# Optimization experiments

Measured on AMD Instinct MI355X. Metric: run time of the kernel, lower is better.

## Reference

```python
import jax, jax.numpy as jnp
import numpy as np

N_NODES = 100000
N_EDGES = 1600000


def setup_inputs() -> dict:
    key = jax.random.key(0)
    k1, k2, k3, k4 = jax.random.split(key, 4)
    x = jax.random.normal(k1, (N_NODES, 16), dtype=jnp.float32)
    edge_index = jax.random.randint(k2, (2, N_EDGES), 0, N_NODES, dtype=jnp.int32)
    # Glorot-ish init for the two GCN layers
    W1 = jax.random.normal(k3, (16, 32), dtype=jnp.float32) * (1.0 / np.sqrt(16))
    b1 = jnp.zeros((32,), dtype=jnp.float32)
    W2 = jax.random.normal(k4, (32, 2), dtype=jnp.float32) * (1.0 / np.sqrt(32))
    b2 = jnp.zeros((2,), dtype=jnp.float32)
    return {"x": x, "edge_index": edge_index, "W1": W1, "b1": b1, "W2": W2, "b2": b2}


def _gcn_conv(x, W, b, src, dst, norm, n_nodes):
    # PyG GCNConv: h = X @ W; aggregate norm * h[src] at dst; add bias.
    h = x @ W                                   # [N, out]
    msg = h[src] * norm[:, None]                # [E+N, out] gather + scale
    out = jax.ops.segment_sum(msg, dst, num_segments=n_nodes)
    return out + b


def reference(x, edge_index, W1, b1, W2, b2):
    n = x.shape[0]
    self_loops = jnp.arange(n, dtype=edge_index.dtype)
    src = jnp.concatenate([edge_index[0], self_loops])  # [E+N]
    dst = jnp.concatenate([edge_index[1], self_loops])
    # Symmetric GCN normalization: deg computed on graph with self-loops
    deg = jax.ops.segment_sum(jnp.ones_like(dst, dtype=x.dtype), dst, num_segments=n)
    dis = jnp.where(deg > 0, jax.lax.rsqrt(deg), 0.0)   # deg^{-1/2}
    norm = dis[src] * dis[dst]                          # [E+N]

    h = jax.nn.relu(_gcn_conv(x, W1, b1, src, dst, norm, n))
    out = _gcn_conv(h, W2, b2, src, dst, norm, n)
    return out
```

## Files before the change

kernel.cpp:

```cpp
#include <hip/hip_runtime.h>
#include <hip/hip_fp16.h>

static constexpr int N  = 100000;
static constexpr int E  = 1600000;
static constexpr int B  = 256;

static constexpr int NBLK  = 250;
static constexpr int CHUNK = E / NBLK;
static constexpr int PERT  = CHUNK / B;
static constexpr int NBUCK = (N + 63) / 64;
static constexpr int NCNT  = NBUCK * NBLK;
static constexpr int NSB   = (NCNT + B - 1) / B;
static constexpr int CAPD1 = 1536;
static constexpr int CAPD2 = 2560;
static constexpr int ROFS_SZ = NBUCK * 64 + 80;

__device__ __forceinline__ int gbase(const int* scanned, const int* bsum, int idx) {
    return scanned[idx] + bsum[idx >> 8];
}


__global__ void kA_hist(const int* __restrict__ dst, int* __restrict__ counts) {
    __shared__ int hist[NBUCK];
    int t = threadIdx.x, blk = blockIdx.x;
    for (int i = t; i < NBUCK; i += B) hist[i] = 0;
    __syncthreads();
    int eb = blk * CHUNK;
#pragma unroll
    for (int k = 0; k < PERT; ++k) {
        int d = dst[eb + k * B + t];
        atomicAdd(&hist[d >> 6], 1);
    }
    __syncthreads();
    for (int b = t; b < NBUCK; b += B) counts[b * NBLK + blk] = hist[b];
}


__global__ void ks1(const int* __restrict__ counts, int* __restrict__ scanned,
                    int* __restrict__ bsum) {
    __shared__ int s[B];
    int t = threadIdx.x;
    int g = blockIdx.x * B + t;
    s[t] = (g < NCNT) ? counts[g] : 0;
    __syncthreads();
    for (int off = 1; off < B; off <<= 1) {
        int v = (t >= off) ? s[t - off] : 0;
        __syncthreads();
        s[t] += v;
        __syncthreads();
    }
    if (g < NCNT) scanned[g] = (t == 0) ? 0 : s[t - 1];
    if (t == B - 1) bsum[blockIdx.x] = s[t];
}

__global__ void ks2(int* __restrict__ bsum) {
    __shared__ int s[1024];
    __shared__ int carry_s;
    int t = threadIdx.x;
    if (t == 0) carry_s = 0;
    __syncthreads();
    for (int base = 0; base < NSB; base += 1024) {
        int idx = base + t;
        s[t] = (idx < NSB) ? bsum[idx] : 0;
        __syncthreads();
        for (int off = 1; off < 1024; off <<= 1) {
            int u = (t >= off) ? s[t - off] : 0;
            __syncthreads();
            s[t] += u;
            __syncthreads();
        }
        int carry = carry_s;
        __syncthreads();
        if (idx < NSB) bsum[idx] = carry + ((t == 0) ? 0 : s[t - 1]);
        if (t == 1023) carry_s = carry + s[1023];
        __syncthreads();
    }
}


__global__ void kC_scatter(const int* __restrict__ src, const int* __restrict__ dst,
                           const int* __restrict__ scanned, const int* __restrict__ bsum,
                           int* __restrict__ packed) {
    __shared__ int lbase[NBUCK];
    __shared__ int cnt2[NBUCK];
    __shared__ int gb[NBUCK];
    __shared__ int partial[B];
    __shared__ int stage[CHUNK];

    int t = threadIdx.x, blk = blockIdx.x;
    for (int i = t; i < NBUCK; i += B) { lbase[i] = 0; cnt2[i] = 0; }
    __syncthreads();

    int eb = blk * CHUNK;
    int ds[PERT], ss[PERT];
#pragma unroll
    for (int k = 0; k < PERT; ++k) {
        int e = eb + k * B + t;
        ds[k] = dst[e];
        ss[k] = src[e];
        atomicAdd(&lbase[ds[k] >> 6], 1);
    }
    __syncthreads();

    int v[8];
    {
        int i0 = 8 * t, sum = 0;
#pragma unroll
        for (int k = 0; k < 8; ++k) {
            v[k] = (i0 + k < NBUCK) ? lbase[i0 + k] : 0;
            sum += v[k];
        }
        partial[t] = sum;
    }
    __syncthreads();
    for (int off = 1; off < B; off <<= 1) {
        int u = (t >= off) ? partial[t - off] : 0;
        __syncthreads();
        partial[t] += u;
        __syncthreads();
    }
    {
        int run = (t == 0) ? 0 : partial[t - 1];
        int i0 = 8 * t;
#pragma unroll
        for (int k = 0; k < 8; ++k) {
            if (i0 + k < NBUCK) lbase[i0 + k] = run;
            run += v[k];
        }
    }
    for (int b = t; b < NBUCK; b += B)
        gb[b] = gbase(scanned, bsum, b * NBLK + blk);
    __syncthreads();

#pragma unroll
    for (int k = 0; k < PERT; ++k) {
        int d = ds[k], b = d >> 6;
        int r = atomicAdd(&cnt2[b], 1);
        stage[lbase[b] + r] = ss[k] | ((d & 63) << 17);
    }
    __syncthreads();

    for (int slot = t; slot < CHUNK; slot += B) {
        int b = 0;
        for (int step = 1024; step; step >>= 1) {
            int nb = b + step;
            if (nb < NBUCK && lbase[nb] <= slot) b = nb;
        }
        packed[gb[b] + (slot - lbase[b])] = stage[slot];
    }
}


__global__ void kD1_sort(const int* __restrict__ packed, const int* __restrict__ scanned,
                         const int* __restrict__ bsum, const float4* __restrict__ x4,
                         int* __restrict__ sorted, int* __restrict__ rofs,
                         __half* __restrict__ xpre) {
    __shared__ int c[64], basec[64], cur[64];
    __shared__ int stage2[CAPD1];
    int t = threadIdx.x, b = blockIdx.x;
    if (t < 64) { c[t] = 0; cur[t] = 0; }
    __syncthreads();

    int e0 = gbase(scanned, bsum, b * NBLK);
    int e1 = (b == NBUCK - 1) ? E : gbase(scanned, bsum, (b + 1) * NBLK);
    int ne = e1 - e0;

    for (int e = e0 + t; e < e1; e += B)
        atomicAdd(&c[packed[e] >> 17], 1);
    __syncthreads();

    if (t < 64) basec[t] = c[t];
    __syncthreads();
    for (int off = 1; off < 64; off <<= 1) {
        int u = (t < 64 && t >= off) ? basec[t - off] : 0;
        __syncthreads();
        if (t < 64) basec[t] += u;
        __syncthreads();
    }
    if (t < 64) basec[t] -= c[t];
    __syncthreads();

    if (ne <= CAPD1) {
        for (int e = e0 + t; e < e1; e += B) {
            int p = packed[e];
            int lo = p >> 17;
            int r = atomicAdd(&cur[lo], 1);
            stage2[basec[lo] + r] = p;
        }
        __syncthreads();
        for (int k = t; k < ne; k += B) sorted[e0 + k] = stage2[k];
    } else {
        for (int e = e0 + t; e < e1; e += B) {
            int p = packed[e];
            int lo = p >> 17;
            int r = atomicAdd(&cur[lo], 1);
            sorted[e0 + basec[lo] + r] = p;
        }
    }

    if (t < 64) rofs[(size_t)b * 64 + t] = e0 + basec[t];
    if (b == NBUCK - 1 && t < 80) rofs[NBUCK * 64 + t] = E;

    int nbase = b * 64;
    {
        int n = t >> 2, j = t & 3;
        int node = nbase + n;
        if (node < N) {
            float d = rsqrtf((float)(c[n] + 1));
            float4 vv = x4[(size_t)node * 4 + j];
            ushort4 pk;
            pk.x = __half_as_ushort(__float2half(vv.x * d));
            pk.y = __half_as_ushort(__float2half(vv.y * d));
            pk.z = __half_as_ushort(__float2half(vv.z * d));
            pk.w = __half_as_ushort(__float2half(vv.w * d));
            *(ushort4*)(xpre + (size_t)node * 16 + j * 4) = pk;
        }
    }
}


__global__ void kD2_agg(const __half* __restrict__ xpre, const int* __restrict__ sorted,
                        const int* __restrict__ rofs, const float* __restrict__ W1,
                        const float* __restrict__ b1, const float* __restrict__ W2,
                        float2* __restrict__ hpre) {
    __shared__ float acc[128 * 17];
    __shared__ float sW1[512], sb1[32], sW2[64];
    __shared__ int stageE[CAPD2];
    int t = threadIdx.x;
    int nb0 = blockIdx.x * 128;
    for (int i = t; i < 512; i += B) sW1[i] = W1[i];
    if (t < 32) sb1[t] = b1[t];
    if (t < 64) sW2[t] = W2[t];

    int r0 = rofs[nb0];
    int rend = rofs[nb0 + 128];
    int rlen = rend - r0;
    bool useL = (rlen <= CAPD2);
    if (useL) for (int k = t; k < rlen; k += B) stageE[k] = sorted[r0 + k];
    __syncthreads();

    int nl = t >> 1, h = t & 1;
    int n = nb0 + nl;
    if (n < N) {
        int rs = rofs[n], re = rofs[n + 1];
        float a0, a1, a2, a3, a4, a5, a6, a7;
        {
            int4 w = *(const int4*)(xpre + (size_t)n * 16 + h * 8);
            float2 q0 = __half22float2(*(__half2*)&w.x);
            float2 q1 = __half22float2(*(__half2*)&w.y);
            float2 q2 = __half22float2(*(__half2*)&w.z);
            float2 q3 = __half22float2(*(__half2*)&w.w);
            a0 = q0.x; a1 = q0.y; a2 = q1.x; a3 = q1.y;
            a4 = q2.x; a5 = q2.y; a6 = q3.x; a7 = q3.y;
        }
        auto add8 = [&](int4 w) {
            float2 q0 = __half22float2(*(__half2*)&w.x);
            float2 q1 = __half22float2(*(__half2*)&w.y);
            float2 q2 = __half22float2(*(__half2*)&w.z);
            float2 q3 = __half22float2(*(__half2*)&w.w);
            a0 += q0.x; a1 += q0.y; a2 += q1.x; a3 += q1.y;
            a4 += q2.x; a5 += q2.y; a6 += q3.x; a7 += q3.y;
        };
        int k = rs;
        for (; k + 4 <= re; k += 4) {
            int w0, w1, w2, w3;
            if (useL) {
                w0 = stageE[k - r0]; w1 = stageE[k + 1 - r0];
                w2 = stageE[k + 2 - r0]; w3 = stageE[k + 3 - r0];
            } else {
                w0 = sorted[k]; w1 = sorted[k + 1];
                w2 = sorted[k + 2]; w3 = sorted[k + 3];
            }
            int4 v0 = *(const int4*)(xpre + (size_t)(w0 & 0x1FFFF) * 16 + h * 8);
            int4 v1 = *(const int4*)(xpre + (size_t)(w1 & 0x1FFFF) * 16 + h * 8);
            int4 v2 = *(const int4*)(xpre + (size_t)(w2 & 0x1FFFF) * 16 + h * 8);
            int4 v3 = *(const int4*)(xpre + (size_t)(w3 & 0x1FFFF) * 16 + h * 8);
            add8(v0); add8(v1); add8(v2); add8(v3);
        }
        for (; k < re; ++k) {
            int w = useL ? stageE[k - r0] : sorted[k];
            add8(*(const int4*)(xpre + (size_t)(w & 0x1FFFF) * 16 + h * 8));
        }
        float* row = acc + nl * 17 + h * 8;
        row[0] = a0; row[1] = a1; row[2] = a2; row[3] = a3;
        row[4] = a4; row[5] = a5; row[6] = a6; row[7] = a7;
    }
    __syncthreads();

    if (t < 128) {
        int n2 = nb0 + t;
        if (n2 < N) {
            int deg = rofs[n2 + 1] - rofs[n2];
            float d = rsqrtf((float)(deg + 1));
            const float* row = acc + t * 17;
            float xi[16];
#pragma unroll
            for (int k = 0; k < 16; ++k) xi[k] = row[k] * d;
            float o0 = 0.f, o1 = 0.f;
#pragma unroll
            for (int c = 0; c < 32; ++c) {
                float hh = sb1[c];
#pragma unroll
                for (int k = 0; k < 16; ++k) hh = fmaf(xi[k], sW1[k * 32 + c], hh);
                hh = fmaxf(hh, 0.f);
                o0 = fmaf(hh, sW2[c * 2 + 0], o0);
                o1 = fmaf(hh, sW2[c * 2 + 1], o1);
            }
            hpre[n2] = make_float2(d * o0, d * o1);
        }
    }
}


__global__ void kF_l2(const float2* __restrict__ hpre, const int* __restrict__ sorted,
                      const int* __restrict__ rofs, const float* __restrict__ b2,
                      float2* __restrict__ out) {
    int n = blockIdx.x * B + threadIdx.x;
    if (n >= N) return;
    int rs = rofs[n], re = rofs[n + 1];
    float2 self = hpre[n];
    float o0 = self.x, o1 = self.y;
    int k = rs;
    for (; k + 4 <= re; k += 4) {
        int w0 = sorted[k], w1 = sorted[k + 1], w2 = sorted[k + 2], w3 = sorted[k + 3];
        float2 v0 = hpre[w0 & 0x1FFFF];
        float2 v1 = hpre[w1 & 0x1FFFF];
        float2 v2 = hpre[w2 & 0x1FFFF];
        float2 v3 = hpre[w3 & 0x1FFFF];
        o0 += (v0.x + v1.x) + (v2.x + v3.x);
        o1 += (v0.y + v1.y) + (v2.y + v3.y);
    }
    for (; k < re; ++k) {
        float2 v = hpre[sorted[k] & 0x1FFFF];
        o0 += v.x; o1 += v.y;
    }
    float d = rsqrtf((float)(re - rs + 1));
    out[n] = make_float2(fmaf(d, o0, b2[0]), fmaf(d, o1, b2[1]));
}


extern "C" void kernel_launch(void* const* d_in, const int* in_sizes, int n_in,
                              void* d_out, int out_size, void* d_ws, size_t ws_size,
                              hipStream_t stream) {
    const float* x  = (const float*)d_in[0];
    const int*   ei = (const int*)d_in[1];
    const float* W1 = (const float*)d_in[2];
    const float* b1 = (const float*)d_in[3];
    const float* W2 = (const float*)d_in[4];
    const float* b2 = (const float*)d_in[5];

    const int* src = ei;
    const int* dst = ei + E;

    int*    packed  = (int*)d_ws;
    int*    sorted  = packed + E;
    int*    counts  = sorted + E;
    int*    scanned = counts + (size_t)NSB * B;
    int*    bsum    = scanned + (size_t)NSB * B;
    int*    rofs    = bsum + 2048;
    float*  hpre    = (float*)(rofs + 100112);
    __half* xpre    = (__half*)(hpre + 2 * (size_t)N);

    kA_hist<<<NBLK, B, 0, stream>>>(dst, counts);
    ks1<<<NSB, B, 0, stream>>>(counts, scanned, bsum);
    ks2<<<1, 1024, 0, stream>>>(bsum);
    kC_scatter<<<NBLK, B, 0, stream>>>(src, dst, scanned, bsum, packed);
    kD1_sort<<<NBUCK, B, 0, stream>>>(packed, scanned, bsum, (const float4*)x,
                                      sorted, rofs, xpre);
    kD2_agg<<<(NBUCK + 1) / 2, B, 0, stream>>>(xpre, sorted, rofs, W1, b1, W2,
                                               (float2*)hpre);
    kF_l2<<<(N + B - 1) / B, B, 0, stream>>>((const float2*)hpre, sorted, rofs, b2,
                                             (float2*)d_out);
}
```

Before: 153.5 us.

## Replace scan-based bucket sort with fixed-capacity slabs and atomic cursors

Result: faster. 131.4 us (-14.4%).

```diff
diff --git a/kernel.cpp b/kernel.cpp
--- a/kernel.cpp
+++ b/kernel.cpp
@@ -7,113 +7,43 @@
 
 static constexpr int NBLK  = 250;
 static constexpr int CHUNK = E / NBLK;
-static constexpr int PERT  = CHUNK / B;
+static constexpr int BC    = 1024;
 static constexpr int NBUCK = (N + 63) / 64;
-static constexpr int NCNT  = NBUCK * NBLK;
-static constexpr int NSB   = (NCNT + B - 1) / B;
-static constexpr int CAPD1 = 1536;
-static constexpr int CAPD2 = 2560;
-static constexpr int ROFS_SZ = NBUCK * 64 + 80;
-
-__device__ __forceinline__ int gbase(const int* scanned, const int* bsum, int idx) {
-    return scanned[idx] + bsum[idx >> 8];
-}
-
-
-__global__ void kA_hist(const int* __restrict__ dst, int* __restrict__ counts) {
-    __shared__ int hist[NBUCK];
+static constexpr int SLAB  = 1536;
+
+
+__global__ __launch_bounds__(BC, 2) void kC_scatter(
+        const int* __restrict__ src, const int* __restrict__ dst,
+        int* __restrict__ gcur, int* __restrict__ gslab) {
+    __shared__ int lhist[NBUCK];
+    __shared__ int lbase[NBUCK];
+    __shared__ int gb[NBUCK];
+    __shared__ int partial[BC];
+    __shared__ int stage[CHUNK];
+
     int t = threadIdx.x, blk = blockIdx.x;
-    for (int i = t; i < NBUCK; i += B) hist[i] = 0;
-    __syncthreads();
+    for (int i = t; i < NBUCK; i += BC) lhist[i] = 0;
+    __syncthreads();
+
     int eb = blk * CHUNK;
-#pragma unroll
-    for (int k = 0; k < PERT; ++k) {
-        int d = dst[eb + k * B + t];
-        atomicAdd(&hist[d >> 6], 1);
-    }
-    __syncthreads();
-    for (int b = t; b < NBUCK; b += B) counts[b * NBLK + blk] = hist[b];
-}
-
-
-__global__ void ks1(const int* __restrict__ counts, int* __restrict__ scanned,
-                    int* __restrict__ bsum) {
-    __shared__ int s[B];
-    int t = threadIdx.x;
-    int g = blockIdx.x * B + t;
-    s[t] = (g < NCNT) ? counts[g] : 0;
-    __syncthreads();
-    for (int off = 1; off < B; off <<= 1) {
-        int v = (t >= off) ? s[t - off] : 0;
-        __syncthreads();
-        s[t] += v;
-        __syncthreads();
-    }
-    if (g < NCNT) scanned[g] = (t == 0) ? 0 : s[t - 1];
-    if (t == B - 1) bsum[blockIdx.x] = s[t];
-}
-
-__global__ void ks2(int* __restrict__ bsum) {
-    __shared__ int s[1024];
-    __shared__ int carry_s;
-    int t = threadIdx.x;
-    if (t == 0) carry_s = 0;
-    __syncthreads();
-    for (int base = 0; base < NSB; base += 1024) {
-        int idx = base + t;
-        s[t] = (idx < NSB) ? bsum[idx] : 0;
-        __syncthreads();
-        for (int off = 1; off < 1024; off <<= 1) {
-            int u = (t >= off) ? s[t - off] : 0;
-            __syncthreads();
-            s[t] += u;
-            __syncthreads();
-        }
-        int carry = carry_s;
-        __syncthreads();
-        if (idx < NSB) bsum[idx] = carry + ((t == 0) ? 0 : s[t - 1]);
-        if (t == 1023) carry_s = carry + s[1023];
-        __syncthreads();
-    }
-}
-
-
-__global__ void kC_scatter(const int* __restrict__ src, const int* __restrict__ dst,
-                           const int* __restrict__ scanned, const int* __restrict__ bsum,
-                           int* __restrict__ packed) {
-    __shared__ int lbase[NBUCK];
-    __shared__ int cnt2[NBUCK];
-    __shared__ int gb[NBUCK];
-    __shared__ int partial[B];
-    __shared__ int stage[CHUNK];
-
-    int t = threadIdx.x, blk = blockIdx.x;
-    for (int i = t; i < NBUCK; i += B) { lbase[i] = 0; cnt2[i] = 0; }
-    __syncthreads();
-
-    int eb = blk * CHUNK;
-    int ds[PERT], ss[PERT];
-#pragma unroll
-    for (int k = 0; k < PERT; ++k) {
-        int e = eb + k * B + t;
-        ds[k] = dst[e];
-        ss[k] = src[e];
-        atomicAdd(&lbase[ds[k] >> 6], 1);
-    }
-    __syncthreads();
-
-    int v[8];
-    {
-        int i0 = 8 * t, sum = 0;
-#pragma unroll
-        for (int k = 0; k < 8; ++k) {
-            v[k] = (i0 + k < NBUCK) ? lbase[i0 + k] : 0;
-            sum += v[k];
-        }
-        partial[t] = sum;
-    }
-    __syncthreads();
-    for (int off = 1; off < B; off <<= 1) {
+    int ds[7], ss[7];
+#pragma unroll
+    for (int k = 0; k < 7; ++k) {
+        int idx = k * BC + t;
+        if (idx < CHUNK) {
+            ds[k] = dst[eb + idx];
+            ss[k] = src[eb + idx];
+            atomicAdd(&lhist[ds[k] >> 6], 1);
+        }
+    }
+    __syncthreads();
+
+    int i0 = 2 * t;
+    int v0 = (i0 < NBUCK) ? lhist[i0] : 0;
+    int v1 = (i0 + 1 < NBUCK) ? lhist[i0 + 1] : 0;
+    partial[t] = v0 + v1;
+    __syncthreads();
+    for (int off = 1; off < BC; off <<= 1) {
         int u = (t >= off) ? partial[t - off] : 0;
         __syncthreads();
         partial[t] += u;
@@ -121,52 +51,54 @@
     }
     {
         int run = (t == 0) ? 0 : partial[t - 1];
-        int i0 = 8 * t;
-#pragma unroll
-        for (int k = 0; k < 8; ++k) {
-            if (i0 + k < NBUCK) lbase[i0 + k] = run;
-            run += v[k];
-        }
-    }
-    for (int b = t; b < NBUCK; b += B)
-        gb[b] = gbase(scanned, bsum, b * NBLK + blk);
-    __syncthreads();
-
-#pragma unroll
-    for (int k = 0; k < PERT; ++k) {
-        int d = ds[k], b = d >> 6;
-        int r = atomicAdd(&cnt2[b], 1);
-        stage[lbase[b] + r] = ss[k] | ((d & 63) << 17);
-    }
-    __syncthreads();
-
-    for (int slot = t; slot < CHUNK; slot += B) {
+        if (i0 < NBUCK) lbase[i0] = run;
+        if (i0 + 1 < NBUCK) lbase[i0 + 1] = run + v0;
+    }
+    for (int bb = t; bb < NBUCK; bb += BC) {
+        int h = lhist[bb];
+        if (h > 0) gb[bb] = bb * SLAB + atomicAdd(&gcur[bb], h);
+        lhist[bb] = 0;
+    }
+    __syncthreads();
+
+#pragma unroll
+    for (int k = 0; k < 7; ++k) {
+        int idx = k * BC + t;
+        if (idx < CHUNK) {
+            int d = ds[k], b = d >> 6;
+            int r = atomicAdd(&lhist[b], 1);
+            stage[lbase[b] + r] = ss[k] | ((d & 63) << 17);
+        }
+    }
+    __syncthreads();
+
+    for (int slot = t; slot < CHUNK; slot += BC) {
         int b = 0;
         for (int step = 1024; step; step >>= 1) {
             int nb = b + step;
             if (nb < NBUCK && lbase[nb] <= slot) b = nb;
         }
-        packed[gb[b] + (slot - lbase[b])] = stage[slot];
-    }
-}
-
-
-__global__ void kD1_sort(const int* __restrict__ packed, const int* __restrict__ scanned,
-                         const int* __restrict__ bsum, const float4* __restrict__ x4,
-                         int* __restrict__ sorted, int* __restrict__ rofs,
+        gslab[gb[b] + (slot - lbase[b])] = stage[slot];
+    }
+}
+
+
+__global__ void kD1_sort(const int* __restrict__ gcur, int* __restrict__ gslab,
+                         int* __restrict__ rofs, const float4* __restrict__ x4,
                          __half* __restrict__ xpre) {
+    __shared__ int st0[SLAB], st1[SLAB];
     __shared__ int c[64], basec[64], cur[64];
-    __shared__ int stage2[CAPD1];
     int t = threadIdx.x, b = blockIdx.x;
     if (t < 64) { c[t] = 0; cur[t] = 0; }
     __syncthreads();
 
-    int e0 = gbase(scanned, bsum, b * NBLK);
-    int e1 = (b == NBUCK - 1) ? E : gbase(scanned, bsum, (b + 1) * NBLK);
-    int ne = e1 - e0;
-
-    for (int e = e0 + t; e < e1; e += B)
-        atomicAdd(&c[packed[e] >> 17], 1);
+    int ne = gcur[b]; if (ne > SLAB) ne = SLAB;
+    int base = b * SLAB;
+    for (int k = t; k < ne; k += B) {
+        int p = gslab[base + k];
+        st0[k] = p;
+        atomicAdd(&c[p >> 17], 1);
+    }
     __syncthreads();
 
     if (t < 64) basec[t] = c[t];
@@ -180,69 +112,50 @@
     if (t < 64) basec[t] -= c[t];
     __syncthreads();
 
-    if (ne <= CAPD1) {
-        for (int e = e0 + t; e < e1; e += B) {
-            int p = packed[e];
-            int lo = p >> 17;
-            int r = atomicAdd(&cur[lo], 1);
-            stage2[basec[lo] + r] = p;
-        }
-        __syncthreads();
-        for (int k = t; k < ne; k += B) sorted[e0 + k] = stage2[k];
-    } else {
-        for (int e = e0 + t; e < e1; e += B) {
-            int p = packed[e];
-            int lo = p >> 17;
-            int r = atomicAdd(&cur[lo], 1);
-            sorted[e0 + basec[lo] + r] = p;
-        }
-    }
-
-    if (t < 64) rofs[(size_t)b * 64 + t] = e0 + basec[t];
-    if (b == NBUCK - 1 && t < 80) rofs[NBUCK * 64 + t] = E;
-
-    int nbase = b * 64;
-    {
-        int n = t >> 2, j = t & 3;
-        int node = nbase + n;
-        if (node < N) {
-            float d = rsqrtf((float)(c[n] + 1));
-            float4 vv = x4[(size_t)node * 4 + j];
-            ushort4 pk;
-            pk.x = __half_as_ushort(__float2half(vv.x * d));
-            pk.y = __half_as_ushort(__float2half(vv.y * d));
-            pk.z = __half_as_ushort(__float2half(vv.z * d));
-            pk.w = __half_as_ushort(__float2half(vv.w * d));
-            *(ushort4*)(xpre + (size_t)node * 16 + j * 4) = pk;
-        }
-    }
-}
-
-
-__global__ void kD2_agg(const __half* __restrict__ xpre, const int* __restrict__ sorted,
+    for (int k = t; k < ne; k += B) {
+        int p = st0[k];
+        int lo = p >> 17;
+        int r = atomicAdd(&cur[lo], 1);
+        st1[basec[lo] + r] = p;
+    }
+    __syncthreads();
+    for (int k = t; k < ne; k += B) gslab[base + k] = st1[k];
+
+    if (t < 64) rofs[b * 65 + t] = base + basec[t];
+    if (t == 64) rofs[b * 65 + 64] = base + ne;
+
+    int n = t >> 2, j = t & 3;
+    int node = b * 64 + n;
+    if (node < N) {
+        float d = rsqrtf((float)(c[n] + 1));
+        float4 vv = x4[(size_t)node * 4 + j];
+        ushort4 pk;
+        pk.x = __half_as_ushort(__float2half(vv.x * d));
+        pk.y = __half_as_ushort(__float2half(vv.y * d));
+        pk.z = __half_as_ushort(__float2half(vv.z * d));
+        pk.w = __half_as_ushort(__float2half(vv.w * d));
+        *(ushort4*)(xpre + (size_t)node * 16 + j * 4) = pk;
+    }
+}
+
+
+__global__ void kD2_agg(const __half* __restrict__ xpre, const int* __restrict__ gslab,
                         const int* __restrict__ rofs, const float* __restrict__ W1,
                         const float* __restrict__ b1, const float* __restrict__ W2,
                         float2* __restrict__ hpre) {
     __shared__ float acc[128 * 17];
     __shared__ float sW1[512], sb1[32], sW2[64];
-    __shared__ int stageE[CAPD2];
     int t = threadIdx.x;
     int nb0 = blockIdx.x * 128;
     for (int i = t; i < 512; i += B) sW1[i] = W1[i];
     if (t < 32) sb1[t] = b1[t];
     if (t < 64) sW2[t] = W2[t];
 
-    int r0 = rofs[nb0];
-    int rend = rofs[nb0 + 128];
-    int rlen = rend - r0;
-    bool useL = (rlen <= CAPD2);
-    if (useL) for (int k = t; k < rlen; k += B) stageE[k] = sorted[r0 + k];
-    __syncthreads();
-
     int nl = t >> 1, h = t & 1;
     int n = nb0 + nl;
     if (n < N) {
-        int rs = rofs[n], re = rofs[n + 1];
+        int bb = n >> 6, lo = n & 63;
+        int rs = rofs[bb * 65 + lo], re = rofs[bb * 65 + lo + 1];
         float a0, a1, a2, a3, a4, a5, a6, a7;
         {
             int4 w = *(const int4*)(xpre + (size_t)n * 16 + h * 8);
@@ -263,24 +176,15 @@
         };
         int k = rs;
         for (; k + 4 <= re; k += 4) {
-            int w0, w1, w2, w3;
-            if (useL) {
-                w0 = stageE[k - r0]; w1 = stageE[k + 1 - r0];
-                w2 = stageE[k + 2 - r0]; w3 = stageE[k + 3 - r0];
-            } else {
-                w0 = sorted[k]; w1 = sorted[k + 1];
-                w2 = sorted[k + 2]; w3 = sorted[k + 3];
-            }
+            int w0 = gslab[k], w1 = gslab[k + 1], w2 = gslab[k + 2], w3 = gslab[k + 3];
             int4 v0 = *(const int4*)(xpre + (size_t)(w0 & 0x1FFFF) * 16 + h * 8);
             int4 v1 = *(const int4*)(xpre + (size_t)(w1 & 0x1FFFF) * 16 + h * 8);
             int4 v2 = *(const int4*)(xpre + (size_t)(w2 & 0x1FFFF) * 16 + h * 8);
             int4 v3 = *(const int4*)(xpre + (size_t)(w3 & 0x1FFFF) * 16 + h * 8);
             add8(v0); add8(v1); add8(v2); add8(v3);
         }
-        for (; k < re; ++k) {
-            int w = useL ? stageE[k - r0] : sorted[k];
-            add8(*(const int4*)(xpre + (size_t)(w & 0x1FFFF) * 16 + h * 8));
-        }
+        for (; k < re; ++k)
+            add8(*(const int4*)(xpre + (size_t)(gslab[k] & 0x1FFFF) * 16 + h * 8));
         float* row = acc + nl * 17 + h * 8;
         row[0] = a0; row[1] = a1; row[2] = a2; row[3] = a3;
         row[4] = a4; row[5] = a5; row[6] = a6; row[7] = a7;
@@ -290,7 +194,8 @@
     if (t < 128) {
         int n2 = nb0 + t;
         if (n2 < N) {
-            int deg = rofs[n2 + 1] - rofs[n2];
+            int bb = n2 >> 6, lo = n2 & 63;
+            int deg = rofs[bb * 65 + lo + 1] - rofs[bb * 65 + lo];
             float d = rsqrtf((float)(deg + 1));
             const float* row = acc + t * 17;
             float xi[16];
@@ -312,17 +217,18 @@
 }
 
 
-__global__ void kF_l2(const float2* __restrict__ hpre, const int* __restrict__ sorted,
+__global__ void kF_l2(const float2* __restrict__ hpre, const int* __restrict__ gslab,
                       const int* __restrict__ rofs, const float* __restrict__ b2,
                       float2* __restrict__ out) {
     int n = blockIdx.x * B + threadIdx.x;
     if (n >= N) return;
-    int rs = rofs[n], re = rofs[n + 1];
+    int bb = n >> 6, lo = n & 63;
+    int rs = rofs[bb * 65 + lo], re = rofs[bb * 65 + lo + 1];
     float2 self = hpre[n];
     float o0 = self.x, o1 = self.y;
     int k = rs;
     for (; k + 4 <= re; k += 4) {
-        int w0 = sorted[k], w1 = sorted[k + 1], w2 = sorted[k + 2], w3 = sorted[k + 3];
+        int w0 = gslab[k], w1 = gslab[k + 1], w2 = gslab[k + 2], w3 = gslab[k + 3];
         float2 v0 = hpre[w0 & 0x1FFFF];
         float2 v1 = hpre[w1 & 0x1FFFF];
         float2 v2 = hpre[w2 & 0x1FFFF];
@@ -331,7 +237,7 @@
         o1 += (v0.y + v1.y) + (v2.y + v3.y);
     }
     for (; k < re; ++k) {
-        float2 v = hpre[sorted[k] & 0x1FFFF];
+        float2 v = hpre[gslab[k] & 0x1FFFF];
         o0 += v.x; o1 += v.y;
     }
     float d = rsqrtf((float)(re - rs + 1));
@@ -352,23 +258,17 @@
     const int* src = ei;
     const int* dst = ei + E;
 
-    int*    packed  = (int*)d_ws;
-    int*    sorted  = packed + E;
-    int*    counts  = sorted + E;
-    int*    scanned = counts + (size_t)NSB * B;
-    int*    bsum    = scanned + (size_t)NSB * B;
-    int*    rofs    = bsum + 2048;
-    float*  hpre    = (float*)(rofs + 100112);
-    __half* xpre    = (__half*)(hpre + 2 * (size_t)N);
-
-    kA_hist<<<NBLK, B, 0, stream>>>(dst, counts);
-    ks1<<<NSB, B, 0, stream>>>(counts, scanned, bsum);
-    ks2<<<1, 1024, 0, stream>>>(bsum);
-    kC_scatter<<<NBLK, B, 0, stream>>>(src, dst, scanned, bsum, packed);
-    kD1_sort<<<NBUCK, B, 0, stream>>>(packed, scanned, bsum, (const float4*)x,
-                                      sorted, rofs, xpre);
-    kD2_agg<<<(NBUCK + 1) / 2, B, 0, stream>>>(xpre, sorted, rofs, W1, b1, W2,
+    int*    gslab = (int*)d_ws;
+    int*    rofs  = gslab + (size_t)NBUCK * SLAB;
+    int*    gcur  = rofs + 101600;
+    float*  hpre  = (float*)(gcur + 1600);
+    __half* xpre  = (__half*)(hpre + 2 * (size_t)N);
+
+    hipMemsetAsync(gcur, 0, NBUCK * sizeof(int), stream);
+    kC_scatter<<<NBLK, BC, 0, stream>>>(src, dst, gcur, gslab);
+    kD1_sort<<<NBUCK, B, 0, stream>>>(gcur, gslab, rofs, (const float4*)x, xpre);
+    kD2_agg<<<(N + 127) / 128, B, 0, stream>>>(xpre, gslab, rofs, W1, b1, W2,
                                                (float2*)hpre);
-    kF_l2<<<(N + B - 1) / B, B, 0, stream>>>((const float2*)hpre, sorted, rofs, b2,
+    kF_l2<<<(N + B - 1) / B, B, 0, stream>>>((const float2*)hpre, gslab, rofs, b2,
                                              (float2*)d_out);
 }
```
